# Kernel tuning notes

Measured on AMD Instinct MI355X. Metric: run time of the kernel, lower is better.

## Reference

```python
import jax, jax.numpy as jnp
import numpy as np

N_NODES = 50000
C = 128
E = 800000
B = 4096
NEG = 5
NUM_LAYERS = 3


def setup_inputs() -> dict:
    key = jax.random.key(0)
    ks = jax.random.split(key, 8)
    edge_index = jax.random.randint(ks[0], (2, E), 0, N_NODES, dtype=jnp.int64)
    edge_weight = jax.random.uniform(ks[1], (E,), dtype=jnp.float32)
    n_id = jax.random.randint(ks[2], ((2 + NEG) * B,), 0, N_NODES, dtype=jnp.int64)
    x = jnp.zeros((1,), jnp.float32)  # ignored by forward (overwritten by id_embed)
    id_embed = jax.random.normal(ks[3], (N_NODES, C), jnp.float32) * 0.1
    w1 = jax.random.normal(ks[4], (2 * C, C), jnp.float32) * (1.0 / np.sqrt(2 * C))
    b1 = jnp.zeros((C,), jnp.float32)
    w2 = jax.random.normal(ks[5], (C, 1), jnp.float32) * (1.0 / np.sqrt(C))
    b2 = jnp.zeros((1,), jnp.float32)
    return {"x": x, "edge_index": edge_index, "edge_weight": edge_weight,
            "n_id": n_id, "neg_sample_num": NEG, "id_embed": id_embed,
            "w1": w1, "b1": b1, "w2": w2, "b2": b2}


def reference(x, edge_index, edge_weight, n_id, neg_sample_num, id_embed, w1, b1, w2, b2):
    n_nodes = id_embed.shape[0]
    row, col = edge_index[0], edge_index[1]
    # symmetric GCN normalization (LGCConv)
    deg = jax.ops.segment_sum(jnp.ones_like(row, dtype=id_embed.dtype), row,
                              num_segments=n_nodes)
    dinv = jnp.where(deg > 0, jax.lax.rsqrt(jnp.maximum(deg, 1e-12)), 0.0)
    norm = (dinv[row] * dinv[col])[:, None]  # [E,1]
    h = id_embed
    final = id_embed
    for _ in range(NUM_LAYERS):
        h = jax.ops.segment_sum(norm * h[col], row, num_segments=n_nodes)
        final = final + h
    final = final / (NUM_LAYERS + 1)
    # split n_id into (out, pos, neg) index groups
    b = n_id.shape[0] // (2 + neg_sample_num)
    out = final[n_id[:b]]
    pos = final[n_id[b:2 * b]]
    neg = final[n_id[2 * b:]]
    tiled_out = jnp.repeat(out, neg_sample_num, axis=0)  # [b*neg, C]

    def pred_head(z):  # Linear -> LeakyReLU(0.2) -> (Dropout eval=identity) -> Linear
        z = jax.nn.leaky_relu(z @ w1 + b1, negative_slope=0.2)
        return z @ w2 + b2

    pos_logit = pred_head(jnp.concatenate([out, pos], axis=-1))
    neg_logits = pred_head(jnp.concatenate([tiled_out, neg], axis=-1))
    return pos_logit, neg_logits
```

## Files before the change

kernel.cpp:

```cpp
#include <hip/hip_runtime.h>
#include <hip/hip_bf16.h>

#define C 128
#define NBKT 128
#define BCAP 8192

typedef __bf16 bf16x8 __attribute__((ext_vector_type(8)));
typedef float floatx4 __attribute__((ext_vector_type(4)));

__device__ __forceinline__ unsigned short f2bf(float f) {
    unsigned u = __float_as_uint(f);
    unsigned r = (u + 0x7FFFu + ((u >> 16) & 1u)) >> 16;
    return (unsigned short)r;
}
__device__ __forceinline__ float bflo(unsigned v) { return __uint_as_float(v << 16); }
__device__ __forceinline__ float bfhi(unsigned v) { return __uint_as_float(v & 0xFFFF0000u); }
__device__ __forceinline__ unsigned packbf(float lo, float hi) {
    return (unsigned)f2bf(lo) | ((unsigned)f2bf(hi) << 16);
}

__device__ __forceinline__ int g_idx(const void* p, long long i, int is64) {
    if (is64) return (int)((const long long*)p)[i];
    return ((const int*)p)[i];
}
__device__ __forceinline__ float g_flt(const void* p, long long i, int isf32) {
    if (isf32) return ((const float*)p)[i];
    return __uint_as_float(((unsigned)((const unsigned short*)p)[i]) << 16);
}

__global__ void k_bucketA(const void* edge, int E, int rpb,
                          unsigned* __restrict__ bucketbuf, int* __restrict__ bucketcnt) {
    __shared__ int lcnt[NBKT];
    __shared__ int lbase[NBKT];
    __shared__ int sflag;
    int t = threadIdx.x;
    if (t < 64) {
        const unsigned* wrd = (const unsigned*)edge;
        int predA = (t < 32) ? (wrd[2 * t + 1] == 0u) : 1;
        unsigned long long mA = __ballot(predA);
        if (t == 0) sflag = (mA == ~0ull) ? 1 : 0;
    }
    __syncthreads();
    int is64 = sflag;
    const int PER = 8;
    int chunkSz = blockDim.x * PER;
    long long stride = (long long)gridDim.x * chunkSz;
    for (long long base = (long long)blockIdx.x * chunkSz; base < E; base += stride) {
        if (t < NBKT) lcnt[t] = 0;
        __syncthreads();
        int bkt[PER], rank[PER];
        unsigned enc[PER];
        long long e0 = base + (long long)t * PER;
        int rr[PER], cc[PER];
        if (e0 + PER <= E) {
            if (is64) {
                const long long* pr = (const long long*)edge + e0;
                const long long* pc = (const long long*)edge + E + e0;
#pragma unroll
                for (int j = 0; j < PER; j += 2) {
                    longlong2 vr = *(const longlong2*)(pr + j);
                    longlong2 vc = *(const longlong2*)(pc + j);
                    rr[j] = (int)vr.x; rr[j + 1] = (int)vr.y;
                    cc[j] = (int)vc.x; cc[j + 1] = (int)vc.y;
                }
            } else {
                const int* pr = (const int*)edge + e0;
                const int* pc = (const int*)edge + E + e0;
#pragma unroll
                for (int j = 0; j < PER; j += 4) {
                    int4 vr = *(const int4*)(pr + j);
                    int4 vc = *(const int4*)(pc + j);
                    rr[j] = vr.x; rr[j + 1] = vr.y; rr[j + 2] = vr.z; rr[j + 3] = vr.w;
                    cc[j] = vc.x; cc[j + 1] = vc.y; cc[j + 2] = vc.z; cc[j + 3] = vc.w;
                }
            }
#pragma unroll
            for (int j = 0; j < PER; ++j) {
                int b = rr[j] / rpb;
                bkt[j] = b;
                enc[j] = ((unsigned)(rr[j] - b * rpb) << 16) | (unsigned)(cc[j] & 0xFFFF);
                rank[j] = atomicAdd(&lcnt[b], 1);
            }
        } else {
#pragma unroll
            for (int j = 0; j < PER; ++j) {
                long long e = e0 + j;
                if (e < E) {
                    int r = g_idx(edge, e, is64);
                    int c = g_idx(edge, (long long)E + e, is64);
                    int b = r / rpb;
                    bkt[j] = b;
                    enc[j] = ((unsigned)(r - b * rpb) << 16) | (unsigned)(c & 0xFFFF);
                    rank[j] = atomicAdd(&lcnt[b], 1);
                } else bkt[j] = -1;
            }
        }
        __syncthreads();
        if (t < NBKT) lbase[t] = atomicAdd(&bucketcnt[t], lcnt[t]);
        __syncthreads();
#pragma unroll
        for (int j = 0; j < PER; ++j) {
            if (bkt[j] >= 0) {
                int pos = lbase[bkt[j]] + rank[j];
                if (pos < BCAP)
                    bucketbuf[(size_t)bkt[j] * BCAP + pos] = enc[j];
            }
        }
    }
}

__global__ __launch_bounds__(512) void k_bsort(
        const unsigned* __restrict__ bucketbuf, const int* __restrict__ bucketcnt,
        int* __restrict__ rowptr, float* __restrict__ dinv, float* __restrict__ di2,
        float* __restrict__ rdinv, unsigned short* __restrict__ cols16, int N, int rpb) {
    __shared__ int hist[512];
    int b = blockIdx.x;
    int t = threadIdx.x;
    int base = 0, cnt = 0, total = 0;
    for (int i = 0; i < NBKT; ++i) {
        int v = bucketcnt[i];
        if (v > BCAP) v = BCAP;
        if (i < b) base += v;
        if (i == b) cnt = v;
        total += v;
    }
    int r0 = b * rpb;
    int rows = N - r0;
    if (rows > rpb) rows = rpb;
    if (rows < 0) rows = 0;

    hist[t] = 0;
    __syncthreads();
    const unsigned* buf = bucketbuf + (size_t)b * BCAP;
    for (int i = t; i < cnt; i += 512) atomicAdd(&hist[buf[i] >> 16], 1);
    __syncthreads();
    int v = hist[t];
    __syncthreads();
    for (int off = 1; off < 512; off <<= 1) {
        int x = (t >= off) ? hist[t - off] : 0;
        __syncthreads();
        hist[t] += x;
        __syncthreads();
    }
    int excl = hist[t] - v;
    if (t < rows) {
        int r = r0 + t;
        rowptr[r] = base + excl;
        float fd = (float)v;
        float dv = (v > 0) ? rsqrtf(fd) : 0.0f;
        dinv[r] = dv;
        di2[r] = dv * dv;
        rdinv[r] = (v > 0) ? sqrtf(fd) : 0.0f;
    }
    if (b == NBKT - 1 && t == 0) {
        rowptr[N] = total;
        dinv[N] = 0.f;
    }
    __syncthreads();
    hist[t] = base + excl;
    __syncthreads();
    for (int i = t; i < cnt; i += 512) {
        unsigned u = buf[i];
        int pos = atomicAdd(&hist[u >> 16], 1);
        cols16[pos] = (unsigned short)(u & 0xFFFF);
    }
}

__global__ void k_initprep(const void* emb,
                           unsigned* __restrict__ h0, unsigned* __restrict__ g1,
                           unsigned* __restrict__ g2, int n2, int SST,
                           const void* w1, const void* b1, const void* w2, const void* b2,
                           unsigned short* __restrict__ w1t, float* __restrict__ b1f,
                           float* __restrict__ w2f, float* __restrict__ b2f) {
    __shared__ int sf32;
    int t = threadIdx.x;
    if (t < 64) {
        const unsigned short* h = (const unsigned short*)emb;
        int ex = (h[2 * t] >> 7) & 0xFF;
        unsigned long long mP = __ballot(ex >= 0x6C && ex <= 0x7F);
        if (t == 0) sf32 = (__popcll(mP) < 32) ? 1 : 0;
    }
    __syncthreads();
    int f32 = sf32;
    int i = blockIdx.x * blockDim.x + t;
    if (i < n2) {
        float lo = g_flt(emb, 2LL * i, f32);
        float hi = g_flt(emb, 2LL * i + 1, f32);
        int n = i >> 6, w = i & 63;
        size_t o = (size_t)(w >> 5) * SST + (size_t)n * 32 + (w & 31);
        h0[o] = packbf(lo, hi);
    }
    if (i < 256 * 128) {
        int k = i >> 7, n = i & 127;
        w1t[n * 256 + k] = f2bf(g_flt(w1, i, f32));
    }
    if (i < 128) {
        b1f[i] = g_flt(b1, i, f32);
        w2f[i] = g_flt(w2, i, f32);
    }
    if (i == 0) b2f[0] = g_flt(b2, 0, f32);
    if (i < 64) {
        int s = i >> 5, w = i & 31;
        size_t o = (size_t)s * SST + (size_t)(n2 >> 6) * 32 + w;
        h0[o] = 0u; g1[o] = 0u; g2[o] = 0u;
    }
}

template<bool SC>
__global__ void k_layer_t(const int* __restrict__ rowptr, const unsigned short* __restrict__ cols16,
                          const uint4* __restrict__ gin, uint4* __restrict__ gout,
                          const float* __restrict__ dsc, const float* __restrict__ di2,
                          int N, int SSTU4) {
    int b = blockIdx.x;
    int slice = (b >> 2) & 1;
    int tile = ((b >> 3) << 2) | (b & 3);
    int node = tile * 32 + (threadIdx.x >> 3);
    if (node >= N) return;
    int l8 = threadIdx.x & 7;
    const uint4* gs = gin + (size_t)slice * SSTU4;
    int p = rowptr[node];
    int end = rowptr[node + 1];
    float a0 = 0.f, a1 = 0.f, a2 = 0.f, a3 = 0.f;
    float a4 = 0.f, a5 = 0.f, a6 = 0.f, a7 = 0.f;
    for (int base = p; base < end; base += 8) {
        int c[8];
#pragma unroll
        for (int j = 0; j < 8; ++j) {
            int idx = base + j;
            int cv = cols16[idx];
            c[j] = (idx < end) ? cv : N;
        }
#pragma unroll
        for (int j = 0; j < 8; ++j) {
            uint4 v = gs[(size_t)c[j] * 8 + l8];
            if (SC) {
                float dc = dsc[c[j]];
                a0 = fmaf(dc, bflo(v.x), a0); a1 = fmaf(dc, bfhi(v.x), a1);
                a2 = fmaf(dc, bflo(v.y), a2); a3 = fmaf(dc, bfhi(v.y), a3);
                a4 = fmaf(dc, bflo(v.z), a4); a5 = fmaf(dc, bfhi(v.z), a5);
                a6 = fmaf(dc, bflo(v.w), a6); a7 = fmaf(dc, bfhi(v.w), a7);
            } else {
                a0 += bflo(v.x); a1 += bfhi(v.x);
                a2 += bflo(v.y); a3 += bfhi(v.y);
                a4 += bflo(v.z); a5 += bfhi(v.z);
                a6 += bflo(v.w); a7 += bfhi(v.w);
            }
        }
    }
    float s = di2[node];
    uint4 o;
    o.x = packbf(a0 * s, a1 * s);
    o.y = packbf(a2 * s, a3 * s);
    o.z = packbf(a4 * s, a5 * s);
    o.w = packbf(a6 * s, a7 * s);
    gout[(size_t)slice * SSTU4 + (size_t)node * 8 + l8] = o;
}

__global__ void k_layer3(const int* __restrict__ rowptr, const unsigned short* __restrict__ cols16,
                         const uint4* __restrict__ gin , const uint4* __restrict__ h0,
                         const uint4* __restrict__ g1, uint4* __restrict__ fin,
                         const float* __restrict__ di2, const float* __restrict__ rdinv,
                         int N, int SSTU4) {
    int b = blockIdx.x;
    int slice = (b >> 2) & 1;
    int tile = ((b >> 3) << 2) | (b & 3);
    int node = tile * 32 + (threadIdx.x >> 3);
    if (node >= N) return;
    int l8 = threadIdx.x & 7;
    size_t sb = (size_t)slice * SSTU4;
    const uint4* gs = gin + sb;
    int p = rowptr[node];
    int end = rowptr[node + 1];
    float a0 = 0.f, a1 = 0.f, a2 = 0.f, a3 = 0.f;
    float a4 = 0.f, a5 = 0.f, a6 = 0.f, a7 = 0.f;
    for (int base = p; base < end; base += 8) {
        int c[8];
#pragma unroll
        for (int j = 0; j < 8; ++j) {
            int idx = base + j;
            int cv = cols16[idx];
            c[j] = (idx < end) ? cv : N;
        }
#pragma unroll
        for (int j = 0; j < 8; ++j) {
            uint4 v = gs[(size_t)c[j] * 8 + l8];
            a0 += bflo(v.x); a1 += bfhi(v.x);
            a2 += bflo(v.y); a3 += bfhi(v.y);
            a4 += bflo(v.z); a5 += bfhi(v.z);
            a6 += bflo(v.w); a7 += bfhi(v.w);
        }
    }
    float s = di2[node];
    float rd = rdinv[node];
    size_t ro = (size_t)node * 8 + l8;
    uint4 x0 = h0[sb + ro];
    uint4 x1 = g1[sb + ro];
    uint4 x2 = gs[ro];
    uint4 o;
    o.x = packbf(0.25f * (bflo(x0.x) + rd * (bflo(x1.x) + bflo(x2.x) + s * a0)),
                 0.25f * (bfhi(x0.x) + rd * (bfhi(x1.x) + bfhi(x2.x) + s * a1)));
    o.y = packbf(0.25f * (bflo(x0.y) + rd * (bflo(x1.y) + bflo(x2.y) + s * a2)),
                 0.25f * (bfhi(x0.y) + rd * (bfhi(x1.y) + bfhi(x2.y) + s * a3)));
    o.z = packbf(0.25f * (bflo(x0.z) + rd * (bflo(x1.z) + bflo(x2.z) + s * a4)),
                 0.25f * (bfhi(x0.z) + rd * (bfhi(x1.z) + bfhi(x2.z) + s * a5)));
    o.w = packbf(0.25f * (bflo(x0.w) + rd * (bflo(x1.w) + bflo(x2.w) + s * a6)),
                 0.25f * (bfhi(x0.w) + rd * (bfhi(x1.w) + bfhi(x2.w) + s * a7)));
    fin[(size_t)node * 16 + slice * 8 + l8] = o;
}

__global__ void k_head(const uint4* __restrict__ fin, const void* n_id,
                       const unsigned short* __restrict__ w1t,
                       const float* __restrict__ b1f, const float* __restrict__ w2f,
                       const float* __restrict__ b2f,
                       float* __restrict__ out, int B, int NEG) {
    __shared__ unsigned short z[64][264];
    __shared__ int sid;
    int t = threadIdx.x;
    if (t < 64) {
        const unsigned* nw = (const unsigned*)n_id;
        int predB = (t < 32) ? (nw[2 * t + 1] == 0u) : 1;
        unsigned long long mB = __ballot(predB);
        if (t == 0) sid = (mB == ~0ull) ? 1 : 0;
    }
    __syncthreads();
    int id64 = sid;
    int mbase = blockIdx.x * 64;

#pragma unroll
    for (int i = 0; i < 8; ++i) {
        int flat = i * 256 + t;
        int m = flat >> 5;
        int q = flat & 31;
        int gm = mbase + m;
        int r;
        if (gm < B) {
            r = (q < 16) ? g_idx(n_id, gm, id64) : g_idx(n_id, B + gm, id64);
        } else {
            int j = gm - B;
            r = (q < 16) ? g_idx(n_id, j / NEG, id64) : g_idx(n_id, 2 * B + j, id64);
        }
        uint4 v = fin[(size_t)r * 16 + (q & 15)];
        *(uint4*)((char*)&z[m][0] + q * 16) = v;
    }
    __syncthreads();

    int wave = t >> 6, lane = t & 63;
    int quad = lane >> 4, l16 = lane & 15;

    floatx4 acc[8] = {};
    bf16x8 a[8];
    const unsigned short* zrow = &z[wave * 16 + l16][0];
#pragma unroll
    for (int ks = 0; ks < 8; ++ks)
        a[ks] = *(const bf16x8*)(zrow + ks * 32 + quad * 8);

#pragma unroll
    for (int ks = 0; ks < 8; ++ks) {
#pragma unroll
        for (int nt = 0; nt < 8; ++nt) {
            bf16x8 b = *(const bf16x8*)(w1t + (nt * 16 + l16) * 256 + ks * 32 + quad * 8);
            acc[nt] = __builtin_amdgcn_mfma_f32_16x16x32_bf16(a[ks], b, acc[nt], 0, 0, 0);
        }
    }

    float s0 = 0.f, s1 = 0.f, s2 = 0.f, s3 = 0.f;
#pragma unroll
    for (int nt = 0; nt < 8; ++nt) {
        int col = nt * 16 + l16;
        float bb = b1f[col], ww = w2f[col];
        float v0 = acc[nt][0] + bb; v0 = (v0 > 0.f) ? v0 : 0.2f * v0; s0 += v0 * ww;
        float v1 = acc[nt][1] + bb; v1 = (v1 > 0.f) ? v1 : 0.2f * v1; s1 += v1 * ww;
        float v2 = acc[nt][2] + bb; v2 = (v2 > 0.f) ? v2 : 0.2f * v2; s2 += v2 * ww;
        float v3 = acc[nt][3] + bb; v3 = (v3 > 0.f) ? v3 : 0.2f * v3; s3 += v3 * ww;
    }
#pragma unroll
    for (int off = 1; off <= 8; off <<= 1) {
        s0 += __shfl_xor(s0, off, 64);
        s1 += __shfl_xor(s1, off, 64);
        s2 += __shfl_xor(s2, off, 64);
        s3 += __shfl_xor(s3, off, 64);
    }
    if (l16 == 0) {
        int rowbase = mbase + wave * 16 + quad * 4;
        float bb2 = b2f[0];
        out[rowbase + 0] = s0 + bb2;
        out[rowbase + 1] = s1 + bb2;
        out[rowbase + 2] = s2 + bb2;
        out[rowbase + 3] = s3 + bb2;
    }
}

extern "C" void kernel_launch(void* const* d_in, const int* in_sizes, int n_in,
                              void* d_out, int out_size, void* d_ws, size_t ws_size,
                              hipStream_t stream) {
    const void* edge_index = d_in[1];
    const void* n_id       = d_in[3];
    const void* id_embed   = d_in[5];
    const void* w1 = d_in[6];
    const void* b1 = d_in[7];
    const void* w2 = d_in[8];
    const void* b2 = d_in[9];
    float* out = (float*)d_out;

    const int E  = in_sizes[1] / 2;
    const int N  = in_sizes[5] / C;
    const int NEG = 5;
    const int B  = in_sizes[3] / (2 + NEG);
    const int n_out_rows = B + B * NEG;
    const int SST = (N + 1) * 32;
    const int SSTU4 = (N + 1) * 8;
    const int NB = 2 * SST;
    const int rpb = (N + NBKT - 1) / NBKT;

    size_t off = 0;
    auto alloc = [&](size_t nf) {
        char* p = (char*)d_ws + off * 4;
        off += (nf + 255) & ~(size_t)255;
        return p;
    };
    int*   bucketcnt = (int*)alloc(NBKT);
    float* dinv      = (float*)alloc(N + 1);
    float* di2       = (float*)alloc(N);
    float* rdinv     = (float*)alloc(N);
    int*   rowptr    = (int*)alloc(N + 1);
    unsigned short* cols16 = (unsigned short*)alloc(((size_t)E + 16 + 1) / 2);
    unsigned* bucketbuf = (unsigned*)alloc((size_t)NBKT * BCAP);
    unsigned* h0     = (unsigned*)alloc(NB);
    unsigned* g1     = (unsigned*)alloc(NB);
    unsigned* g2     = (unsigned*)alloc(NB);
    unsigned* fin    = (unsigned*)alloc((size_t)N * 64);
    unsigned short* w1t = (unsigned short*)alloc(256 * 128 / 2);
    float* b1f       = (float*)alloc(C);
    float* w2f       = (float*)alloc(C);
    float* b2f       = (float*)alloc(8);

    const int BS = 256;
    hipMemsetAsync(bucketcnt, 0, NBKT * sizeof(int), stream);

    const int gridA = (E + BS * 8 - 1) / (BS * 8);
    k_bucketA<<<gridA, BS, 0, stream>>>(edge_index, E, rpb, bucketbuf, bucketcnt);
    k_bsort<<<NBKT, 512, 0, stream>>>(bucketbuf, bucketcnt, rowptr, dinv, di2, rdinv,
                                      cols16, N, rpb);
    k_initprep<<<(N * 64 + BS - 1) / BS, BS, 0, stream>>>(
        id_embed, h0, g1, g2, N * 64, SST, w1, b1, w2, b2, w1t, b1f, w2f, b2f);

    const int tiles = (N + 31) / 32;
    const int layer_grid = 8 * ((tiles + 3) / 4);
    k_layer_t<true><<<layer_grid, BS, 0, stream>>>(rowptr, cols16, (const uint4*)h0,
                                                   (uint4*)g1, dinv, di2, N, SSTU4);
    k_layer_t<false><<<layer_grid, BS, 0, stream>>>(rowptr, cols16, (const uint4*)g1,
                                                    (uint4*)g2, nullptr, di2, N, SSTU4);
    k_layer3<<<layer_grid, BS, 0, stream>>>(rowptr, cols16, (const uint4*)g2, (const uint4*)h0,
                                            (const uint4*)g1, (uint4*)fin, di2, rdinv,
                                            N, SSTU4);

    k_head<<<n_out_rows / 64, BS, 0, stream>>>((const uint4*)fin, n_id, w1t, b1f, w2f, b2f,
                                               out, B, NEG);
}
```

Baseline: 221.7 us.

## Prescale embeddings by dinv and compute final layer only for queried nodes

The initial embedding is now prescaled by dinv in the init kernel, writing a separate g0 buffer, so the first propagation layer becomes a plain sum and no longer gathers a per-neighbour dinv. Nodes referenced by n_id are marked in a byte mask, and the third layer skips every node not in the mask, since only those rows feed the prediction head. The cost is an extra bf16 buffer write in init, a scattered mark pass, and a larger memset to zero the mask. It also drops the dinv[N] sentinel write, which the new path appears not to need.

```diff
diff --git a/kernel.cpp b/kernel.cpp
--- a/kernel.cpp
+++ b/kernel.cpp
@@ -152,10 +152,7 @@
         di2[r] = dv * dv;
         rdinv[r] = (v > 0) ? sqrtf(fd) : 0.0f;
     }
-    if (b == NBKT - 1 && t == 0) {
-        rowptr[N] = total;
-        dinv[N] = 0.f;
-    }
+    if (b == NBKT - 1 && t == 0) rowptr[N] = total;
     __syncthreads();
     hist[t] = base + excl;
     __syncthreads();
@@ -166,22 +163,30 @@
     }
 }
 
-__global__ void k_initprep(const void* emb,
-                           unsigned* __restrict__ h0, unsigned* __restrict__ g1,
-                           unsigned* __restrict__ g2, int n2, int SST,
+__global__ void k_initprep(const void* emb, const float* __restrict__ dinv,
+                           unsigned* __restrict__ h0, unsigned* __restrict__ g0,
+                           unsigned* __restrict__ g1, unsigned* __restrict__ g2,
+                           int n2, int SST,
                            const void* w1, const void* b1, const void* w2, const void* b2,
                            unsigned short* __restrict__ w1t, float* __restrict__ b1f,
-                           float* __restrict__ w2f, float* __restrict__ b2f) {
-    __shared__ int sf32;
+                           float* __restrict__ w2f, float* __restrict__ b2f,
+                           const void* n_id, int nids, unsigned char* __restrict__ mark) {
+    __shared__ int sf32, sid;
     int t = threadIdx.x;
     if (t < 64) {
         const unsigned short* h = (const unsigned short*)emb;
         int ex = (h[2 * t] >> 7) & 0xFF;
         unsigned long long mP = __ballot(ex >= 0x6C && ex <= 0x7F);
-        if (t == 0) sf32 = (__popcll(mP) < 32) ? 1 : 0;
-    }
-    __syncthreads();
-    int f32 = sf32;
+        const unsigned* nw = (const unsigned*)n_id;
+        int predB = (t < 32) ? (nw[2 * t + 1] == 0u) : 1;
+        unsigned long long mB = __ballot(predB);
+        if (t == 0) {
+            sf32 = (__popcll(mP) < 32) ? 1 : 0;
+            sid = (mB == ~0ull) ? 1 : 0;
+        }
+    }
+    __syncthreads();
+    int f32 = sf32, id64 = sid;
     int i = blockIdx.x * blockDim.x + t;
     if (i < n2) {
         float lo = g_flt(emb, 2LL * i, f32);
@@ -189,7 +194,10 @@
         int n = i >> 6, w = i & 63;
         size_t o = (size_t)(w >> 5) * SST + (size_t)n * 32 + (w & 31);
         h0[o] = packbf(lo, hi);
-    }
+        float dv = dinv[n];
+        g0[o] = packbf(lo * dv, hi * dv);
+    }
+    if (i < nids) mark[g_idx(n_id, i, id64)] = 1;
     if (i < 256 * 128) {
         int k = i >> 7, n = i & 127;
         w1t[n * 256 + k] = f2bf(g_flt(w1, i, f32));
@@ -202,15 +210,13 @@
     if (i < 64) {
         int s = i >> 5, w = i & 31;
         size_t o = (size_t)s * SST + (size_t)(n2 >> 6) * 32 + w;
-        h0[o] = 0u; g1[o] = 0u; g2[o] = 0u;
-    }
-}
-
-template<bool SC>
-__global__ void k_layer_t(const int* __restrict__ rowptr, const unsigned short* __restrict__ cols16,
-                          const uint4* __restrict__ gin, uint4* __restrict__ gout,
-                          const float* __restrict__ dsc, const float* __restrict__ di2,
-                          int N, int SSTU4) {
+        g0[o] = 0u; g1[o] = 0u; g2[o] = 0u;
+    }
+}
+
+__global__ void k_layer(const int* __restrict__ rowptr, const unsigned short* __restrict__ cols16,
+                        const uint4* __restrict__ gin, uint4* __restrict__ gout,
+                        const float* __restrict__ di2, int N, int SSTU4) {
     int b = blockIdx.x;
     int slice = (b >> 2) & 1;
     int tile = ((b >> 3) << 2) | (b & 3);
@@ -233,18 +239,10 @@
 #pragma unroll
         for (int j = 0; j < 8; ++j) {
             uint4 v = gs[(size_t)c[j] * 8 + l8];
-            if (SC) {
-                float dc = dsc[c[j]];
-                a0 = fmaf(dc, bflo(v.x), a0); a1 = fmaf(dc, bfhi(v.x), a1);
-                a2 = fmaf(dc, bflo(v.y), a2); a3 = fmaf(dc, bfhi(v.y), a3);
-                a4 = fmaf(dc, bflo(v.z), a4); a5 = fmaf(dc, bfhi(v.z), a5);
-                a6 = fmaf(dc, bflo(v.w), a6); a7 = fmaf(dc, bfhi(v.w), a7);
-            } else {
-                a0 += bflo(v.x); a1 += bfhi(v.x);
-                a2 += bflo(v.y); a3 += bfhi(v.y);
-                a4 += bflo(v.z); a5 += bfhi(v.z);
-                a6 += bflo(v.w); a7 += bfhi(v.w);
-            }
+            a0 += bflo(v.x); a1 += bfhi(v.x);
+            a2 += bflo(v.y); a3 += bfhi(v.y);
+            a4 += bflo(v.z); a5 += bfhi(v.z);
+            a6 += bflo(v.w); a7 += bfhi(v.w);
         }
     }
     float s = di2[node];
@@ -260,12 +258,13 @@
                          const uint4* __restrict__ gin , const uint4* __restrict__ h0,
                          const uint4* __restrict__ g1, uint4* __restrict__ fin,
                          const float* __restrict__ di2, const float* __restrict__ rdinv,
-                         int N, int SSTU4) {
+                         const unsigned char* __restrict__ mark, int N, int SSTU4) {
     int b = blockIdx.x;
     int slice = (b >> 2) & 1;
     int tile = ((b >> 3) << 2) | (b & 3);
     int node = tile * 32 + (threadIdx.x >> 3);
     if (node >= N) return;
+    if (!mark[node]) return;
     int l8 = threadIdx.x & 7;
     size_t sb = (size_t)slice * SSTU4;
     const uint4* gs = gin + sb;
@@ -406,6 +405,7 @@
     const int N  = in_sizes[5] / C;
     const int NEG = 5;
     const int B  = in_sizes[3] / (2 + NEG);
+    const int nids = (2 + NEG) * B;
     const int n_out_rows = B + B * NEG;
     const int SST = (N + 1) * 32;
     const int SSTU4 = (N + 1) * 8;
@@ -419,6 +419,7 @@
         return p;
     };
     int*   bucketcnt = (int*)alloc(NBKT);
+    unsigned char* mark = (unsigned char*)alloc((N + 3) / 4);
     float* dinv      = (float*)alloc(N + 1);
     float* di2       = (float*)alloc(N);
     float* rdinv     = (float*)alloc(N);
@@ -426,6 +427,7 @@
     unsigned short* cols16 = (unsigned short*)alloc(((size_t)E + 16 + 1) / 2);
     unsigned* bucketbuf = (unsigned*)alloc((size_t)NBKT * BCAP);
     unsigned* h0     = (unsigned*)alloc(NB);
+    unsigned* g0     = (unsigned*)alloc(NB);
     unsigned* g1     = (unsigned*)alloc(NB);
     unsigned* g2     = (unsigned*)alloc(NB);
     unsigned* fin    = (unsigned*)alloc((size_t)N * 64);
@@ -435,24 +437,25 @@
     float* b2f       = (float*)alloc(8);
 
     const int BS = 256;
-    hipMemsetAsync(bucketcnt, 0, NBKT * sizeof(int), stream);
+    hipMemsetAsync(bucketcnt, 0, 1024 + (size_t)N, stream);
 
     const int gridA = (E + BS * 8 - 1) / (BS * 8);
     k_bucketA<<<gridA, BS, 0, stream>>>(edge_index, E, rpb, bucketbuf, bucketcnt);
     k_bsort<<<NBKT, 512, 0, stream>>>(bucketbuf, bucketcnt, rowptr, dinv, di2, rdinv,
                                       cols16, N, rpb);
     k_initprep<<<(N * 64 + BS - 1) / BS, BS, 0, stream>>>(
-        id_embed, h0, g1, g2, N * 64, SST, w1, b1, w2, b2, w1t, b1f, w2f, b2f);
+        id_embed, dinv, h0, g0, g1, g2, N * 64, SST, w1, b1, w2, b2,
+        w1t, b1f, w2f, b2f, n_id, nids, mark);
 
     const int tiles = (N + 31) / 32;
     const int layer_grid = 8 * ((tiles + 3) / 4);
-    k_layer_t<true><<<layer_grid, BS, 0, stream>>>(rowptr, cols16, (const uint4*)h0,
-                                                   (uint4*)g1, dinv, di2, N, SSTU4);
-    k_layer_t<false><<<layer_grid, BS, 0, stream>>>(rowptr, cols16, (const uint4*)g1,
-                                                    (uint4*)g2, nullptr, di2, N, SSTU4);
+    k_layer<<<layer_grid, BS, 0, stream>>>(rowptr, cols16, (const uint4*)g0, (uint4*)g1,
+                                           di2, N, SSTU4);
+    k_layer<<<layer_grid, BS, 0, stream>>>(rowptr, cols16, (const uint4*)g1, (uint4*)g2,
+                                           di2, N, SSTU4);
     k_layer3<<<layer_grid, BS, 0, stream>>>(rowptr, cols16, (const uint4*)g2, (const uint4*)h0,
                                             (const uint4*)g1, (uint4*)fin, di2, rdinv,
-                                            N, SSTU4);
+                                            mark, N, SSTU4);
 
     k_head<<<n_out_rows / 64, BS, 0, stream>>>((const uint4*)fin, n_id, w1t, b1f, w2f, b2f,
                                                out, B, NEG);
```

New measurement: 212.6 us. 4.1% less time.
